# Performance work log

Measured on AMD Instinct MI355X. Metric: run time of the kernel, lower is better.

Reference implementation:

```python
import jax, jax.numpy as jnp
import numpy as np

N_NODES = 100000
N_EDGES = 1600000
IN_C, HID_C, OUT_C = 128, 256, 256


def sage_conv(x, src, dst, W_l, b_l, W_r, n_nodes):
    # mean aggregation of source-node features onto destination nodes
    msg_sum = jax.ops.segment_sum(x[src], dst, num_segments=n_nodes)  # [N, F]
    deg = jax.ops.segment_sum(jnp.ones_like(dst, dtype=x.dtype), dst, num_segments=n_nodes)
    aggr = msg_sum / jnp.maximum(deg, 1.0)[:, None]
    # PyG SAGEConv: lin_l(aggr) (with bias) + lin_r(x) (no bias)
    return aggr @ W_l + b_l + x @ W_r


def setup_inputs() -> dict:
    key = jax.random.key(0)
    ks = jax.random.split(key, 12)
    x = jax.random.normal(ks[0], (N_NODES, IN_C), dtype=jnp.float32)
    edge_src = jax.random.randint(ks[1], (N_EDGES,), 0, N_NODES)
    edge_dst = jax.random.randint(ks[2], (N_EDGES,), 0, N_NODES)

    def glorot(k, fan_in, fan_out):
        s = jnp.sqrt(2.0 / (fan_in + fan_out)).astype(jnp.float32)
        return jax.random.normal(k, (fan_in, fan_out), dtype=jnp.float32) * s

    return {
        "x": x,
        "W_l0": glorot(ks[3], IN_C, HID_C), "b_l0": jnp.zeros((HID_C,), jnp.float32),
        "W_r0": glorot(ks[4], IN_C, HID_C),
        "W_l1": glorot(ks[5], HID_C, HID_C), "b_l1": jnp.zeros((HID_C,), jnp.float32),
        "W_r1": glorot(ks[6], HID_C, HID_C),
        "W_l2": glorot(ks[7], HID_C, OUT_C), "b_l2": jnp.zeros((OUT_C,), jnp.float32),
        "W_r2": glorot(ks[8], HID_C, OUT_C),
        "edge_src": edge_src,
        "edge_dst": edge_dst,
    }


def reference(x, W_l0, b_l0, W_r0, W_l1, b_l1, W_r1, W_l2, b_l2, W_r2, edge_src, edge_dst):
    n = x.shape[0]
    h = sage_conv(x, edge_src, edge_dst, W_l0, b_l0, W_r0, n)
    h = jax.nn.relu(h)  # dropout p=0.0 -> identity
    h = sage_conv(h, edge_src, edge_dst, W_l1, b_l1, W_r1, n)
    h = jax.nn.relu(h)
    h = sage_conv(h, edge_src, edge_dst, W_l2, b_l2, W_r2, n)
    return h
```

## Files before the change

kernel.cpp:

```cpp
#include <hip/hip_runtime.h>
#include <cstdint>
#include <cstddef>


#define N_NODES 100000
#define N_EDGES 1600000

#define SCAN_BLOCKS 256
#define SCAN_T 256
#define FILL_PASSES 4

typedef unsigned short ushort;
typedef unsigned int uint;
typedef __attribute__((ext_vector_type(8))) short short8;
typedef __attribute__((ext_vector_type(4))) float floatx4;

#define AS1 __attribute__((address_space(1)))
#define AS3 __attribute__((address_space(3)))

__device__ __forceinline__ float bf2f(ushort h) {
    union { uint u; float f; } c; c.u = ((uint)h) << 16; return c.f;
}
__device__ __forceinline__ ushort f2bf(float f) {
    union { float f; uint u; } c; c.f = f;
    uint u = c.u;
    return (ushort)((u + 0x7FFFu + ((u >> 16) & 1u)) >> 16);
}


__global__ void count_edges(const int* __restrict__ dst, int* __restrict__ cnt) {
    int i = blockIdx.x * blockDim.x + threadIdx.x;
    if (i < N_EDGES) atomicAdd(&cnt[dst[i]], 1);
}

__global__ __launch_bounds__(SCAN_T) void scan_partial(
    const int* __restrict__ cnt, int* __restrict__ bsum, int n)
{
    int chunk = (n + SCAN_BLOCKS - 1) / SCAN_BLOCKS;
    int beg = blockIdx.x * chunk;
    int end = beg + chunk; if (end > n) end = n;
    int t = threadIdx.x;
    int s = 0;
    for (int i = beg + t; i < end; i += SCAN_T) s += cnt[i];
    __shared__ int sh[SCAN_T];
    sh[t] = s;
    __syncthreads();
    for (int off = SCAN_T / 2; off > 0; off >>= 1) {
        if (t < off) sh[t] += sh[t + off];
        __syncthreads();
    }
    if (t == 0) bsum[blockIdx.x] = sh[0];
}

__global__ __launch_bounds__(SCAN_T) void scan_block_sums(int* __restrict__ bsum) {
    int t = threadIdx.x;
    __shared__ int sh[SCAN_T];
    int v = bsum[t];
    sh[t] = v;
    __syncthreads();
    for (int off = 1; off < SCAN_T; off <<= 1) {
        int u = (t >= off) ? sh[t - off] : 0;
        __syncthreads();
        sh[t] += u;
        __syncthreads();
    }
    bsum[t] = sh[t] - v;
}

__global__ __launch_bounds__(SCAN_T) void scan_fill(
    int* __restrict__ cnt, const int* __restrict__ bsum,
    int* __restrict__ row_ptr, int n)
{
    int chunk = (n + SCAN_BLOCKS - 1) / SCAN_BLOCKS;
    int beg = blockIdx.x * chunk;
    int end = beg + chunk; if (end > n) end = n;
    int t = threadIdx.x;
    int per = (chunk + SCAN_T - 1) / SCAN_T;
    int tb = beg + t * per;
    int te = tb + per; if (te > end) te = end;
    int s = 0;
    for (int i = tb; i < te; ++i) s += cnt[i];
    __shared__ int sh[SCAN_T];
    sh[t] = s;
    __syncthreads();
    for (int off = 1; off < SCAN_T; off <<= 1) {
        int u = (t >= off) ? sh[t - off] : 0;
        __syncthreads();
        sh[t] += u;
        __syncthreads();
    }
    int running = bsum[blockIdx.x] + sh[t] - s;
    for (int i = tb; i < te; ++i) {
        int c = cnt[i];
        row_ptr[i] = running;
        cnt[i] = running;
        running += c;
    }
    if (blockIdx.x == 0 && t == 0) row_ptr[n] = N_EDGES;
}

__global__ void fill_csr(const int* __restrict__ src, const int* __restrict__ dst,
                         int* __restrict__ cursor, int* __restrict__ col_idx) {
    int i = blockIdx.x * blockDim.x + threadIdx.x;
    if (i >= N_EDGES) return;
    int lo = (int)blockIdx.y * (N_NODES / FILL_PASSES);
    int hi = lo + (N_NODES / FILL_PASSES);
    int d = dst[i];
    if (d >= lo && d < hi) {
        int p = atomicAdd(&cursor[d], 1);
        col_idx[p] = src[i];
    }
}


__global__ void convert_x_bf16(const float* __restrict__ x, ushort* __restrict__ xb, int n4) {
    int i = blockIdx.x * blockDim.x + threadIdx.x;
    if (i >= n4) return;
    float4 v = *(const float4*)&x[(size_t)i * 4];
    ushort4 o;
    o.x = f2bf(v.x); o.y = f2bf(v.y); o.z = f2bf(v.z); o.w = f2bf(v.w);
    *(ushort4*)&xb[(size_t)i * 4] = o;
}

__global__ void transpose_w_bf16(const float* __restrict__ W, ushort* __restrict__ Wt, int kshift) {
    int i = blockIdx.x * blockDim.x + threadIdx.x;
    int K = 1 << kshift;
    if (i >= 256 * K) return;
    int n = i >> kshift;
    int k = i & (K - 1);
    Wt[i] = f2bf(W[k * 256 + n]);
}

__global__ __launch_bounds__(64) void aggregate_bf16(
    const ushort* __restrict__ xb, const int* __restrict__ row_ptr,
    const int* __restrict__ col_idx, ushort* __restrict__ outb, int F)
{
    int node = blockIdx.x;
    int t = threadIdx.x;
    int b = row_ptr[node], e = row_ptr[node + 1];
    float d = (float)(e - b); if (d < 1.f) d = 1.f;
    float inv = 1.f / d;

    if (F == 256) {
        int c = t * 4;
        float a0 = 0.f, a1 = 0.f, a2 = 0.f, a3 = 0.f;
        float b0 = 0.f, b1 = 0.f, b2 = 0.f, b3 = 0.f;
        int i = b;
        for (; i + 1 < e; i += 2) {
            int s0 = col_idx[i];
            int s1 = col_idx[i + 1];
            uint2 v0 = *(const uint2*)&xb[(size_t)s0 * 256 + c];
            uint2 v1 = *(const uint2*)&xb[(size_t)s1 * 256 + c];
            a0 += bf2f((ushort)(v0.x & 0xffff)); a1 += bf2f((ushort)(v0.x >> 16));
            a2 += bf2f((ushort)(v0.y & 0xffff)); a3 += bf2f((ushort)(v0.y >> 16));
            b0 += bf2f((ushort)(v1.x & 0xffff)); b1 += bf2f((ushort)(v1.x >> 16));
            b2 += bf2f((ushort)(v1.y & 0xffff)); b3 += bf2f((ushort)(v1.y >> 16));
        }
        if (i < e) {
            int s0 = col_idx[i];
            uint2 v0 = *(const uint2*)&xb[(size_t)s0 * 256 + c];
            a0 += bf2f((ushort)(v0.x & 0xffff)); a1 += bf2f((ushort)(v0.x >> 16));
            a2 += bf2f((ushort)(v0.y & 0xffff)); a3 += bf2f((ushort)(v0.y >> 16));
        }
        ushort4 o;
        o.x = f2bf((a0 + b0) * inv); o.y = f2bf((a1 + b1) * inv);
        o.z = f2bf((a2 + b2) * inv); o.w = f2bf((a3 + b3) * inv);
        *(ushort4*)&outb[(size_t)node * 256 + c] = o;
    } else {
        int c = t * 2;
        float a0 = 0.f, a1 = 0.f, b0 = 0.f, b1 = 0.f;
        int i = b;
        for (; i + 1 < e; i += 2) {
            int s0 = col_idx[i];
            int s1 = col_idx[i + 1];
            uint v0 = *(const uint*)&xb[(size_t)s0 * 128 + c];
            uint v1 = *(const uint*)&xb[(size_t)s1 * 128 + c];
            a0 += bf2f((ushort)(v0 & 0xffff)); a1 += bf2f((ushort)(v0 >> 16));
            b0 += bf2f((ushort)(v1 & 0xffff)); b1 += bf2f((ushort)(v1 >> 16));
        }
        if (i < e) {
            int s0 = col_idx[i];
            uint v0 = *(const uint*)&xb[(size_t)s0 * 128 + c];
            a0 += bf2f((ushort)(v0 & 0xffff)); a1 += bf2f((ushort)(v0 >> 16));
        }
        ushort2 o;
        o.x = f2bf((a0 + b0) * inv); o.y = f2bf((a1 + b1) * inv);
        *(ushort2*)&outb[(size_t)node * 128 + c] = o;
    }
}

__global__ __launch_bounds__(512, 4) void gemm_wres(
    const ushort* __restrict__ A1, const ushort* __restrict__ W1t,
    const ushort* __restrict__ A2, const ushort* __restrict__ W2t,
    const float* __restrict__ bias, ushort* __restrict__ out_bf,
    float* __restrict__ out_f32, int M, int K, int relu)
{
    __shared__ __align__(16) ushort Wl[32 * 128 * 8];
    int tid = threadIdx.x;
    int w = tid >> 6, lane = tid & 63;
    int m_ = lane & 15, koq = lane >> 4;
    int c0 = blockIdx.y * 128;
    int row0 = blockIdx.x * 256;
    int KQ = K >> 3;
    int nj = (KQ * 128) >> 9;
    int nk = K >> 5;

    floatx4 acc[2][8];
#pragma unroll
    for (int i = 0; i < 2; ++i)
#pragma unroll
        for (int f = 0; f < 8; ++f) acc[i][f] = (floatx4){0.f, 0.f, 0.f, 0.f};

    int ra = row0 + w * 32 + m_;      if (ra > M - 1) ra = M - 1;
    int rb = row0 + w * 32 + 16 + m_; if (rb > M - 1) rb = M - 1;

    for (int mm = 0; mm < 2; ++mm) {
        const ushort* __restrict__ A  = mm ? A2 : A1;
        const ushort* __restrict__ Wt = mm ? W2t : W1t;
        if (mm) __syncthreads();
        for (int j = 0; j < nj; ++j) {
            int s = j * 512 + tid;
            int q = s >> 7, col = s & 127;
            __builtin_amdgcn_global_load_lds(
                (const AS1 uint*)&Wt[(size_t)(c0 + col) * K + q * 8],
                (AS3 uint*)&Wl[(size_t)(j * 512 + w * 64) * 8], 16, 0, 0);
        }
        __syncthreads();

        const ushort* __restrict__ Aa = &A[(size_t)ra * K + koq * 8];
        const ushort* __restrict__ Ab = &A[(size_t)rb * K + koq * 8];

        short8 a0 = *(const short8*)&Aa[0];
        short8 a1 = *(const short8*)&Ab[0];
        for (int kk = 0; kk < nk; ++kk) {
            short8 n0, n1;
            if (kk + 1 < nk) {
                n0 = *(const short8*)&Aa[(kk + 1) * 32];
                n1 = *(const short8*)&Ab[(kk + 1) * 32];
            }
            const ushort* bbase = &Wl[(size_t)((kk * 4 + koq) * 128 + m_) * 8];
#pragma unroll
            for (int fc = 0; fc < 8; ++fc) {
                short8 b = *(const short8*)&bbase[fc * 128];
                acc[0][fc] = __builtin_amdgcn_mfma_f32_16x16x32_bf16(a0, b, acc[0][fc], 0, 0, 0);
                acc[1][fc] = __builtin_amdgcn_mfma_f32_16x16x32_bf16(a1, b, acc[1][fc], 0, 0, 0);
            }
            a0 = n0; a1 = n1;
        }
    }

#pragma unroll
    for (int m2 = 0; m2 < 2; ++m2) {
#pragma unroll
        for (int fc = 0; fc < 8; ++fc) {
            int col = c0 + fc * 16 + m_;
            float bv = bias[col];
#pragma unroll
            for (int r = 0; r < 4; ++r) {
                int row = row0 + w * 32 + m2 * 16 + koq * 4 + r;
                if (row >= M) continue;
                float v = acc[m2][fc][r] + bv;
                if (relu) v = fmaxf(v, 0.f);
                if (out_f32) out_f32[(size_t)row * 256 + col] = v;
                else         out_bf [(size_t)row * 256 + col] = f2bf(v);
            }
        }
    }
}


extern "C" void kernel_launch(void* const* d_in, const int* in_sizes, int n_in,
                              void* d_out, int out_size, void* d_ws, size_t ws_size,
                              hipStream_t stream) {
    const float* x    = (const float*)d_in[0];
    const float* W_l0 = (const float*)d_in[1];
    const float* b_l0 = (const float*)d_in[2];
    const float* W_r0 = (const float*)d_in[3];
    const float* W_l1 = (const float*)d_in[4];
    const float* b_l1 = (const float*)d_in[5];
    const float* W_r1 = (const float*)d_in[6];
    const float* W_l2 = (const float*)d_in[7];
    const float* b_l2 = (const float*)d_in[8];
    const float* W_r2 = (const float*)d_in[9];
    const int* esrc   = (const int*)d_in[10];
    const int* edst   = (const int*)d_in[11];
    float* out = (float*)d_out;

    size_t off = 0;
    char* ws = (char*)d_ws;
    auto take = [&](size_t bytes) -> void* {
        void* p = ws + off;
        off += (bytes + 255) & ~(size_t)255;
        return p;
    };
    int*    cnt     = (int*)take((size_t)N_NODES * 4);
    int*    row_ptr = (int*)take((size_t)(N_NODES + 1) * 4);
    int*    col_idx = (int*)take((size_t)N_EDGES * 4);
    int*    bsum    = (int*)take((size_t)SCAN_BLOCKS * 4);
    ushort* xb      = (ushort*)take((size_t)N_NODES * 128 * 2);
    ushort* Wl0t    = (ushort*)take((size_t)256 * 128 * 2);
    ushort* Wr0t    = (ushort*)take((size_t)256 * 128 * 2);
    ushort* Wl1t    = (ushort*)take((size_t)256 * 256 * 2);
    ushort* Wr1t    = (ushort*)take((size_t)256 * 256 * 2);
    ushort* Wl2t    = (ushort*)take((size_t)256 * 256 * 2);
    ushort* Wr2t    = (ushort*)take((size_t)256 * 256 * 2);
    ushort* aggrb   = (ushort*)take((size_t)N_NODES * 256 * 2);
    ushort* ha      = (ushort*)take((size_t)N_NODES * 256 * 2);
    ushort* hb      = (ushort*)take((size_t)N_NODES * 256 * 2);
    (void)ws_size; (void)in_sizes; (void)n_in; (void)out_size;

    hipMemsetAsync(cnt, 0, (size_t)N_NODES * 4, stream);
    int eb = (N_EDGES + 255) / 256;
    count_edges<<<eb, 256, 0, stream>>>(edst, cnt);
    scan_partial<<<SCAN_BLOCKS, SCAN_T, 0, stream>>>(cnt, bsum, N_NODES);
    scan_block_sums<<<1, SCAN_T, 0, stream>>>(bsum);
    scan_fill<<<SCAN_BLOCKS, SCAN_T, 0, stream>>>(cnt, bsum, row_ptr, N_NODES);
    fill_csr<<<dim3(eb, FILL_PASSES), 256, 0, stream>>>(esrc, edst, cnt, col_idx);

    int n4 = (N_NODES * 128) / 4;
    convert_x_bf16<<<(n4 + 255) / 256, 256, 0, stream>>>(x, xb, n4);
    transpose_w_bf16<<<(256 * 128 + 255) / 256, 256, 0, stream>>>(W_l0, Wl0t, 7);
    transpose_w_bf16<<<(256 * 128 + 255) / 256, 256, 0, stream>>>(W_r0, Wr0t, 7);
    transpose_w_bf16<<<(256 * 256 + 255) / 256, 256, 0, stream>>>(W_l1, Wl1t, 8);
    transpose_w_bf16<<<(256 * 256 + 255) / 256, 256, 0, stream>>>(W_r1, Wr1t, 8);
    transpose_w_bf16<<<(256 * 256 + 255) / 256, 256, 0, stream>>>(W_l2, Wl2t, 8);
    transpose_w_bf16<<<(256 * 256 + 255) / 256, 256, 0, stream>>>(W_r2, Wr2t, 8);

    dim3 ggrid((N_NODES + 255) / 256, 2);

    aggregate_bf16<<<N_NODES, 64, 0, stream>>>(xb, row_ptr, col_idx, aggrb, 128);
    gemm_wres<<<ggrid, 512, 0, stream>>>(aggrb, Wl0t, xb, Wr0t, b_l0,
                                         ha, nullptr, N_NODES, 128, 1);
    aggregate_bf16<<<N_NODES, 64, 0, stream>>>(ha, row_ptr, col_idx, aggrb, 256);
    gemm_wres<<<ggrid, 512, 0, stream>>>(aggrb, Wl1t, ha, Wr1t, b_l1,
                                         hb, nullptr, N_NODES, 256, 1);
    aggregate_bf16<<<N_NODES, 64, 0, stream>>>(hb, row_ptr, col_idx, aggrb, 256);
    gemm_wres<<<ggrid, 512, 0, stream>>>(aggrb, Wl2t, hb, Wr2t, b_l2,
                                         nullptr, out, N_NODES, 256, 0);
}
```

Measured before the change: 807.8 us.

## Fuse prep kernels, widen aggregation loads, use full-width GEMM tiles

Merges edge counting, x conversion and the six weight transposes into one launch to cut launch overhead. The aggregation kernel now has each half-wave handle alternate edges with 16-byte loads and four gathers in flight, then combines halves with a shuffle. The GEMM computes all 256 output columns per block instead of two 128-column blocks, so each A tile is read once. The cost is twice the LDS and accumulator registers, with launch bounds relaxed to one block per CU, which may lower occupancy.

```diff
diff --git a/kernel.cpp b/kernel.cpp
--- a/kernel.cpp
+++ b/kernel.cpp
@@ -28,10 +28,42 @@
 }
 
 
-__global__ void count_edges(const int* __restrict__ dst, int* __restrict__ cnt) {
+#define N4X (N_NODES * 128 / 4)
+
+__global__ void prep_all(
+    const int* __restrict__ dst, int* __restrict__ cnt,
+    const float* __restrict__ x, ushort* __restrict__ xb,
+    const float* __restrict__ Wl0, ushort* __restrict__ Wl0t,
+    const float* __restrict__ Wr0, ushort* __restrict__ Wr0t,
+    const float* __restrict__ Wl1, ushort* __restrict__ Wl1t,
+    const float* __restrict__ Wr1, ushort* __restrict__ Wr1t,
+    const float* __restrict__ Wl2, ushort* __restrict__ Wl2t,
+    const float* __restrict__ Wr2, ushort* __restrict__ Wr2t)
+{
     int i = blockIdx.x * blockDim.x + threadIdx.x;
-    if (i < N_EDGES) atomicAdd(&cnt[dst[i]], 1);
-}
+    if (i < N_EDGES) { atomicAdd(&cnt[dst[i]], 1); return; }
+    i -= N_EDGES;
+    if (i < N4X) {
+        float4 v = *(const float4*)&x[(size_t)i * 4];
+        ushort4 o;
+        o.x = f2bf(v.x); o.y = f2bf(v.y); o.z = f2bf(v.z); o.w = f2bf(v.w);
+        *(ushort4*)&xb[(size_t)i * 4] = o;
+        return;
+    }
+    i -= N4X;
+    if (i < 32768) { Wl0t[i] = f2bf(Wl0[(i & 127) * 256 + (i >> 7)]); return; }
+    i -= 32768;
+    if (i < 32768) { Wr0t[i] = f2bf(Wr0[(i & 127) * 256 + (i >> 7)]); return; }
+    i -= 32768;
+    if (i < 65536) { Wl1t[i] = f2bf(Wl1[(i & 255) * 256 + (i >> 8)]); return; }
+    i -= 65536;
+    if (i < 65536) { Wr1t[i] = f2bf(Wr1[(i & 255) * 256 + (i >> 8)]); return; }
+    i -= 65536;
+    if (i < 65536) { Wl2t[i] = f2bf(Wl2[(i & 255) * 256 + (i >> 8)]); return; }
+    i -= 65536;
+    if (i < 65536) { Wr2t[i] = f2bf(Wr2[(i & 255) * 256 + (i >> 8)]); return; }
+}
+
 
 __global__ __launch_bounds__(SCAN_T) void scan_partial(
     const int* __restrict__ cnt, int* __restrict__ bsum, int n)
@@ -112,104 +144,120 @@
     }
 }
 
-
-__global__ void convert_x_bf16(const float* __restrict__ x, ushort* __restrict__ xb, int n4) {
-    int i = blockIdx.x * blockDim.x + threadIdx.x;
-    if (i >= n4) return;
-    float4 v = *(const float4*)&x[(size_t)i * 4];
-    ushort4 o;
-    o.x = f2bf(v.x); o.y = f2bf(v.y); o.z = f2bf(v.z); o.w = f2bf(v.w);
-    *(ushort4*)&xb[(size_t)i * 4] = o;
-}
-
-__global__ void transpose_w_bf16(const float* __restrict__ W, ushort* __restrict__ Wt, int kshift) {
-    int i = blockIdx.x * blockDim.x + threadIdx.x;
-    int K = 1 << kshift;
-    if (i >= 256 * K) return;
-    int n = i >> kshift;
-    int k = i & (K - 1);
-    Wt[i] = f2bf(W[k * 256 + n]);
-}
-
 __global__ __launch_bounds__(64) void aggregate_bf16(
     const ushort* __restrict__ xb, const int* __restrict__ row_ptr,
     const int* __restrict__ col_idx, ushort* __restrict__ outb, int F)
 {
     int node = blockIdx.x;
-    int t = threadIdx.x;
+    int lane = threadIdx.x;
+    int half = lane >> 5, li = lane & 31;
     int b = row_ptr[node], e = row_ptr[node + 1];
     float d = (float)(e - b); if (d < 1.f) d = 1.f;
     float inv = 1.f / d;
 
     if (F == 256) {
-        int c = t * 4;
-        float a0 = 0.f, a1 = 0.f, a2 = 0.f, a3 = 0.f;
-        float b0 = 0.f, b1 = 0.f, b2 = 0.f, b3 = 0.f;
+        float a[8];
+#pragma unroll
+        for (int j = 0; j < 8; ++j) a[j] = 0.f;
+        const int c = li * 8;
         int i = b;
+        for (; i + 7 < e; i += 8) {
+            int s0 = col_idx[i + half];
+            int s1 = col_idx[i + 2 + half];
+            int s2 = col_idx[i + 4 + half];
+            int s3 = col_idx[i + 6 + half];
+            uint4 v0 = *(const uint4*)&xb[(size_t)s0 * 256 + c];
+            uint4 v1 = *(const uint4*)&xb[(size_t)s1 * 256 + c];
+            uint4 v2 = *(const uint4*)&xb[(size_t)s2 * 256 + c];
+            uint4 v3 = *(const uint4*)&xb[(size_t)s3 * 256 + c];
+#define ACC4(v) \
+            a[0] += bf2f((ushort)(v.x & 0xffff)); a[1] += bf2f((ushort)(v.x >> 16)); \
+            a[2] += bf2f((ushort)(v.y & 0xffff)); a[3] += bf2f((ushort)(v.y >> 16)); \
+            a[4] += bf2f((ushort)(v.z & 0xffff)); a[5] += bf2f((ushort)(v.z >> 16)); \
+            a[6] += bf2f((ushort)(v.w & 0xffff)); a[7] += bf2f((ushort)(v.w >> 16));
+            ACC4(v0) ACC4(v1) ACC4(v2) ACC4(v3)
+        }
         for (; i + 1 < e; i += 2) {
+            int s0 = col_idx[i + half];
+            uint4 v0 = *(const uint4*)&xb[(size_t)s0 * 256 + c];
+            ACC4(v0)
+        }
+        if (i < e && half == 0) {
             int s0 = col_idx[i];
-            int s1 = col_idx[i + 1];
-            uint2 v0 = *(const uint2*)&xb[(size_t)s0 * 256 + c];
-            uint2 v1 = *(const uint2*)&xb[(size_t)s1 * 256 + c];
-            a0 += bf2f((ushort)(v0.x & 0xffff)); a1 += bf2f((ushort)(v0.x >> 16));
-            a2 += bf2f((ushort)(v0.y & 0xffff)); a3 += bf2f((ushort)(v0.y >> 16));
-            b0 += bf2f((ushort)(v1.x & 0xffff)); b1 += bf2f((ushort)(v1.x >> 16));
-            b2 += bf2f((ushort)(v1.y & 0xffff)); b3 += bf2f((ushort)(v1.y >> 16));
-        }
-        if (i < e) {
+            uint4 v0 = *(const uint4*)&xb[(size_t)s0 * 256 + c];
+            ACC4(v0)
+        }
+#undef ACC4
+#pragma unroll
+        for (int j = 0; j < 8; ++j) a[j] += __shfl(a[j], li + 32);
+        if (half == 0) {
+            short8 o;
+#pragma unroll
+            for (int j = 0; j < 8; ++j) o[j] = (short)f2bf(a[j] * inv);
+            *(short8*)&outb[(size_t)node * 256 + c] = o;
+        }
+    } else {
+        float a[4];
+#pragma unroll
+        for (int j = 0; j < 4; ++j) a[j] = 0.f;
+        const int c = li * 4;
+        int i = b;
+        for (; i + 7 < e; i += 8) {
+            int s0 = col_idx[i + half];
+            int s1 = col_idx[i + 2 + half];
+            int s2 = col_idx[i + 4 + half];
+            int s3 = col_idx[i + 6 + half];
+            uint2 v0 = *(const uint2*)&xb[(size_t)s0 * 128 + c];
+            uint2 v1 = *(const uint2*)&xb[(size_t)s1 * 128 + c];
+            uint2 v2 = *(const uint2*)&xb[(size_t)s2 * 128 + c];
+            uint2 v3 = *(const uint2*)&xb[(size_t)s3 * 128 + c];
+#define ACC2(v) \
+            a[0] += bf2f((ushort)(v.x & 0xffff)); a[1] += bf2f((ushort)(v.x >> 16)); \
+            a[2] += bf2f((ushort)(v.y & 0xffff)); a[3] += bf2f((ushort)(v.y >> 16));
+            ACC2(v0) ACC2(v1) ACC2(v2) ACC2(v3)
+        }
+        for (; i + 1 < e; i += 2) {
+            int s0 = col_idx[i + half];
+            uint2 v0 = *(const uint2*)&xb[(size_t)s0 * 128 + c];
+            ACC2(v0)
+        }
+        if (i < e && half == 0) {
             int s0 = col_idx[i];
-            uint2 v0 = *(const uint2*)&xb[(size_t)s0 * 256 + c];
-            a0 += bf2f((ushort)(v0.x & 0xffff)); a1 += bf2f((ushort)(v0.x >> 16));
-            a2 += bf2f((ushort)(v0.y & 0xffff)); a3 += bf2f((ushort)(v0.y >> 16));
-        }
-        ushort4 o;
-        o.x = f2bf((a0 + b0) * inv); o.y = f2bf((a1 + b1) * inv);
-        o.z = f2bf((a2 + b2) * inv); o.w = f2bf((a3 + b3) * inv);
-        *(ushort4*)&outb[(size_t)node * 256 + c] = o;
-    } else {
-        int c = t * 2;
-        float a0 = 0.f, a1 = 0.f, b0 = 0.f, b1 = 0.f;
-        int i = b;
-        for (; i + 1 < e; i += 2) {
-            int s0 = col_idx[i];
-            int s1 = col_idx[i + 1];
-            uint v0 = *(const uint*)&xb[(size_t)s0 * 128 + c];
-            uint v1 = *(const uint*)&xb[(size_t)s1 * 128 + c];
-            a0 += bf2f((ushort)(v0 & 0xffff)); a1 += bf2f((ushort)(v0 >> 16));
-            b0 += bf2f((ushort)(v1 & 0xffff)); b1 += bf2f((ushort)(v1 >> 16));
-        }
-        if (i < e) {
-            int s0 = col_idx[i];
-            uint v0 = *(const uint*)&xb[(size_t)s0 * 128 + c];
-            a0 += bf2f((ushort)(v0 & 0xffff)); a1 += bf2f((ushort)(v0 >> 16));
-        }
-        ushort2 o;
-        o.x = f2bf((a0 + b0) * inv); o.y = f2bf((a1 + b1) * inv);
-        *(ushort2*)&outb[(size_t)node * 128 + c] = o;
-    }
-}
-
-__global__ __launch_bounds__(512, 4) void gemm_wres(
+            uint2 v0 = *(const uint2*)&xb[(size_t)s0 * 128 + c];
+            ACC2(v0)
+        }
+#undef ACC2
+#pragma unroll
+        for (int j = 0; j < 4; ++j) a[j] += __shfl(a[j], li + 32);
+        if (half == 0) {
+            ushort4 o;
+            o.x = f2bf(a[0] * inv); o.y = f2bf(a[1] * inv);
+            o.z = f2bf(a[2] * inv); o.w = f2bf(a[3] * inv);
+            *(ushort4*)&outb[(size_t)node * 128 + c] = o;
+        }
+    }
+}
+
+__global__ __launch_bounds__(512, 1) void gemm_wres(
     const ushort* __restrict__ A1, const ushort* __restrict__ W1t,
     const ushort* __restrict__ A2, const ushort* __restrict__ W2t,
     const float* __restrict__ bias, ushort* __restrict__ out_bf,
     float* __restrict__ out_f32, int M, int K, int relu)
 {
-    __shared__ __align__(16) ushort Wl[32 * 128 * 8];
+    __shared__ __align__(16) ushort Wl[32 * 256 * 8];
     int tid = threadIdx.x;
     int w = tid >> 6, lane = tid & 63;
     int m_ = lane & 15, koq = lane >> 4;
-    int c0 = blockIdx.y * 128;
     int row0 = blockIdx.x * 256;
     int KQ = K >> 3;
-    int nj = (KQ * 128) >> 9;
+    int nj = (KQ * 256) >> 9;
     int nk = K >> 5;
 
-    floatx4 acc[2][8];
+    floatx4 acc[2][16];
 #pragma unroll
     for (int i = 0; i < 2; ++i)
 #pragma unroll
-        for (int f = 0; f < 8; ++f) acc[i][f] = (floatx4){0.f, 0.f, 0.f, 0.f};
+        for (int f = 0; f < 16; ++f) acc[i][f] = (floatx4){0.f, 0.f, 0.f, 0.f};
 
     int ra = row0 + w * 32 + m_;      if (ra > M - 1) ra = M - 1;
     int rb = row0 + w * 32 + 16 + m_; if (rb > M - 1) rb = M - 1;
@@ -220,9 +268,9 @@
         if (mm) __syncthreads();
         for (int j = 0; j < nj; ++j) {
             int s = j * 512 + tid;
-            int q = s >> 7, col = s & 127;
+            int q = s >> 8, col = s & 255;
             __builtin_amdgcn_global_load_lds(
-                (const AS1 uint*)&Wt[(size_t)(c0 + col) * K + q * 8],
+                (const AS1 uint*)&Wt[(size_t)col * K + q * 8],
                 (AS3 uint*)&Wl[(size_t)(j * 512 + w * 64) * 8], 16, 0, 0);
         }
         __syncthreads();
@@ -238,9 +286,9 @@
                 n0 = *(const short8*)&Aa[(kk + 1) * 32];
                 n1 = *(const short8*)&Ab[(kk + 1) * 32];
             }
-            const ushort* bbase = &Wl[(size_t)((kk * 4 + koq) * 128 + m_) * 8];
-#pragma unroll
-            for (int fc = 0; fc < 8; ++fc) {
+            const ushort* bbase = &Wl[(size_t)((kk * 4 + koq) * 256 + m_) * 8];
+#pragma unroll
+            for (int fc = 0; fc < 16; ++fc) {
                 short8 b = *(const short8*)&bbase[fc * 128];
                 acc[0][fc] = __builtin_amdgcn_mfma_f32_16x16x32_bf16(a0, b, acc[0][fc], 0, 0, 0);
                 acc[1][fc] = __builtin_amdgcn_mfma_f32_16x16x32_bf16(a1, b, acc[1][fc], 0, 0, 0);
@@ -252,8 +300,8 @@
 #pragma unroll
     for (int m2 = 0; m2 < 2; ++m2) {
 #pragma unroll
-        for (int fc = 0; fc < 8; ++fc) {
-            int col = c0 + fc * 16 + m_;
+        for (int fc = 0; fc < 16; ++fc) {
+            int col = fc * 16 + m_;
             float bv = bias[col];
 #pragma unroll
             for (int r = 0; r < 4; ++r) {
@@ -310,23 +358,18 @@
     (void)ws_size; (void)in_sizes; (void)n_in; (void)out_size;
 
     hipMemsetAsync(cnt, 0, (size_t)N_NODES * 4, stream);
-    int eb = (N_EDGES + 255) / 256;
-    count_edges<<<eb, 256, 0, stream>>>(edst, cnt);
+    int total_prep = N_EDGES + N4X + 2 * 32768 + 4 * 65536;
+    prep_all<<<(total_prep + 255) / 256, 256, 0, stream>>>(
+        edst, cnt, x, xb,
+        W_l0, Wl0t, W_r0, Wr0t, W_l1, Wl1t, W_r1, Wr1t, W_l2, Wl2t, W_r2, Wr2t);
+
     scan_partial<<<SCAN_BLOCKS, SCAN_T, 0, stream>>>(cnt, bsum, N_NODES);
     scan_block_sums<<<1, SCAN_T, 0, stream>>>(bsum);
     scan_fill<<<SCAN_BLOCKS, SCAN_T, 0, stream>>>(cnt, bsum, row_ptr, N_NODES);
+    int eb = (N_EDGES + 255) / 256;
     fill_csr<<<dim3(eb, FILL_PASSES), 256, 0, stream>>>(esrc, edst, cnt, col_idx);
 
-    int n4 = (N_NODES * 128) / 4;
-    convert_x_bf16<<<(n4 + 255) / 256, 256, 0, stream>>>(x, xb, n4);
-    transpose_w_bf16<<<(256 * 128 + 255) / 256, 256, 0, stream>>>(W_l0, Wl0t, 7);
-    transpose_w_bf16<<<(256 * 128 + 255) / 256, 256, 0, stream>>>(W_r0, Wr0t, 7);
-    transpose_w_bf16<<<(256 * 256 + 255) / 256, 256, 0, stream>>>(W_l1, Wl1t, 8);
-    transpose_w_bf16<<<(256 * 256 + 255) / 256, 256, 0, stream>>>(W_r1, Wr1t, 8);
-    transpose_w_bf16<<<(256 * 256 + 255) / 256, 256, 0, stream>>>(W_l2, Wl2t, 8);
-    transpose_w_bf16<<<(256 * 256 + 255) / 256, 256, 0, stream>>>(W_r2, Wr2t, 8);
-
-    dim3 ggrid((N_NODES + 255) / 256, 2);
+    dim3 ggrid((N_NODES + 255) / 256, 1);
 
     aggregate_bf16<<<N_NODES, 64, 0, stream>>>(xb, row_ptr, col_idx, aggrb, 128);
     gemm_wres<<<ggrid, 512, 0, stream>>>(aggrb, Wl0t, xb, Wr0t, b_l0,
```

Result: slower. 837.6 us (+3.7%).
